# Kernel tuning notes

Hardware: AMD Instinct MI355X
Metric: run time of the kernel (lower is better)

## Reference

```python
import jax, jax.numpy as jnp
import numpy as np

N = 20000      # nodes
E = 640000     # edges
FIN = 256
FQK = 256


def setup_inputs() -> dict:
    key = jax.random.key(0)
    kx, ks, kd, kw = jax.random.split(key, 4)
    x = jax.random.normal(kx, (N, FIN), dtype=jnp.float32)
    # src must be sorted (original scatter_softmax assumes grouped index);
    # force last element to N-1 so nbatches == N as in batch[-1]+1.
    src = jnp.sort(jax.random.randint(ks, (E,), 0, N))
    src = src.at[-1].set(N - 1)
    dest = jax.random.randint(kd, (E,), 0, N)
    ei = jnp.stack([src, dest]).astype(jnp.int64)
    # nn.Linear(Fin, 2*Fqk, bias=False) weight: [2*Fqk, Fin]
    bound = 1.0 / np.sqrt(FIN)
    W = jax.random.uniform(kw, (2 * FQK, FIN), dtype=jnp.float32,
                           minval=-bound, maxval=bound)
    return {"x": x, "ei": ei, "W": W}


def reference(x, ei, W):
    src, dest = ei[0], ei[1]
    n_nodes = x.shape[0]
    scaling = FQK ** -0.5
    qk = x @ W.T                      # [N, 2*Fqk]
    q, k = jnp.split(qk, 2, axis=-1)  # each [N, Fqk]
    q = q * scaling
    # per-edge dot product: (q[src] . k[dest])  -> [E]
    aw = jnp.einsum('ef,ef->e', q[src], k[dest])
    # scatter softmax over edges grouped by src node (raw exp, as original)
    ex = jnp.exp(aw)
    expsum = jax.ops.segment_sum(ex, src, num_segments=n_nodes)  # [N]
    return ex / expsum[src]
```

## Files before the change

kernel.cpp:

```cpp
#include <hip/hip_runtime.h>
#include <cmath>

#define FIN 256
#define FQK 256
#define SCALING 0.0625f
#define MAX_SEG 256

typedef __bf16 bf16_t;
typedef bf16_t bf16x8 __attribute__((ext_vector_type(8)));
typedef float  f32x4  __attribute__((ext_vector_type(4)));

__device__ __forceinline__ unsigned short f2bf(float f) {
    unsigned int u = __float_as_uint(f);
    u += 0x7FFFu + ((u >> 16) & 1u);
    return (unsigned short)(u >> 16);
}
__device__ __forceinline__ float bf_lo(unsigned int w) { return __uint_as_float(w << 16); }
__device__ __forceinline__ float bf_hi(unsigned int w) { return __uint_as_float(w & 0xFFFF0000u); }
__device__ __forceinline__ unsigned int pack2(float a, float b) {
    return (unsigned int)f2bf(a) | ((unsigned int)f2bf(b) << 16);
}

__global__ __launch_bounds__(256) void prep_wb_kernel(const float* __restrict__ W,
                                                      unsigned int* __restrict__ Wb2) {
    const int i = blockIdx.x * 256 + threadIdx.x;
    const float4 v = *(const float4*)(W + (size_t)i * 4);
    uint2 p;
    p.x = pack2(v.x, v.y);
    p.y = pack2(v.z, v.w);
    *(uint2*)(Wb2 + (size_t)i * 2) = p;
}

#define GROWS    32
#define SAROW    264

__global__ __launch_bounds__(256) void gemm_qk_kernel(const float* __restrict__ x,
                                                      const unsigned short* __restrict__ Wb,
                                                      unsigned short* __restrict__ qarr,
                                                      unsigned short* __restrict__ karr,
                                                      int N) {
    __shared__ unsigned short sA[GROWS * SAROW];

    const int h    = blockIdx.y;
    const unsigned short* __restrict__ Wbh = Wb + (size_t)h * FQK * FIN;
    unsigned short* __restrict__ outp = h ? karr : qarr;
    const float scale = h ? 1.0f : SCALING;

    const int t    = threadIdx.x;
    const int wv   = t >> 6;
    const int lane = t & 63;
    const int q    = lane >> 4;
    const int m16  = lane & 15;
    const int n0   = blockIdx.x * GROWS;
    const int f0   = wv * 64;

    uint4 bfrag[4][8];
#pragma unroll
    for (int ft = 0; ft < 4; ++ft) {
        const unsigned short* __restrict__ brow = Wbh + (size_t)(f0 + ft * 16 + m16) * FIN;
#pragma unroll
        for (int kc = 0; kc < 8; ++kc)
            bfrag[ft][kc] = *(const uint4*)(brow + kc * 32 + q * 8);
    }

    {
        const int r  = t >> 6;
        const int c4 = (t & 63) * 4;
#pragma unroll
        for (int u = 0; u < 8; ++u) {
            const int row = u * 4 + r;
            const int n = n0 + row;
            float4 v = make_float4(0.f, 0.f, 0.f, 0.f);
            if (n < N) v = *(const float4*)(x + (size_t)n * FIN + c4);
            uint2 p;
            p.x = pack2(v.x, v.y);
            p.y = pack2(v.z, v.w);
            *(uint2*)&sA[row * SAROW + c4] = p;
        }
    }
    __syncthreads();

    f32x4 acc[2][4] = {};
#pragma unroll
    for (int kc = 0; kc < 8; ++kc) {
        bf16x8 afrag[2];
#pragma unroll
        for (int mt = 0; mt < 2; ++mt)
            afrag[mt] = *(const bf16x8*)&sA[(mt * 16 + m16) * SAROW + kc * 32 + q * 8];
#pragma unroll
        for (int ft = 0; ft < 4; ++ft) {
            union { uint4 u; bf16x8 v; } bu;
            bu.u = bfrag[ft][kc];
#pragma unroll
            for (int mt = 0; mt < 2; ++mt)
                acc[mt][ft] = __builtin_amdgcn_mfma_f32_16x16x32_bf16(afrag[mt], bu.v,
                                                                     acc[mt][ft], 0, 0, 0);
        }
    }

#pragma unroll
    for (int mt = 0; mt < 2; ++mt) {
#pragma unroll
        for (int r = 0; r < 4; ++r) {
            const int n = n0 + mt * 16 + q * 4 + r;
            if (n < N) {
#pragma unroll
                for (int ft = 0; ft < 4; ++ft)
                    outp[(size_t)n * FIN + f0 + ft * 16 + m16] = f2bf(acc[mt][ft][r] * scale);
            }
        }
    }
}

__global__ __launch_bounds__(256) void seg_kernel(const int* __restrict__ src,
                                                  int* __restrict__ seg, int N, int E) {
    const int n = blockIdx.x * 256 + threadIdx.x;
    if (n > N) return;
    int lo = 0, hi = E;
    while (lo < hi) {
        const int mid = (lo + hi) >> 1;
        if (src[mid] < n) lo = mid + 1; else hi = mid;
    }
    seg[n] = lo;
}

__global__ __launch_bounds__(256) void node_edge_kernel(const unsigned short* __restrict__ qarr,
                                                        const unsigned short* __restrict__ karr,
                                                        const int* __restrict__ dest,
                                                        const int* __restrict__ seg,
                                                        float* __restrict__ out, int N) {
    __shared__ float exlds[4][MAX_SEG];

    const int w    = threadIdx.x >> 6;
    const int lane = threadIdx.x & 63;
    const int n    = blockIdx.x * 4 + w;
    const int g    = lane >> 4;
    const int j    = lane & 15;

    int   s0 = 0, cnt = 0;
    float inv = 0.f;

    if (n < N) {
        s0 = seg[n];
        cnt = seg[n + 1] - s0;
    }

    if (cnt > 0) {
        const uint4* __restrict__ qr = (const uint4*)(qarr + (size_t)n * FIN);
        const uint4 qa0 = qr[j];
        const uint4 qa1 = qr[16 + j];
        float4 xa, xb, xc, xd;
        xa.x = bf_lo(qa0.x); xa.y = bf_hi(qa0.x); xa.z = bf_lo(qa0.y); xa.w = bf_hi(qa0.y);
        xb.x = bf_lo(qa0.z); xb.y = bf_hi(qa0.z); xb.z = bf_lo(qa0.w); xb.w = bf_hi(qa0.w);
        xc.x = bf_lo(qa1.x); xc.y = bf_hi(qa1.x); xc.z = bf_lo(qa1.y); xc.w = bf_hi(qa1.y);
        xd.x = bf_lo(qa1.z); xd.y = bf_hi(qa1.z); xd.z = bf_lo(qa1.w); xd.w = bf_hi(qa1.w);

        float sum = 0.f;
        for (int base = 0; base < cnt; base += 64) {
            const int m = min(64, cnt - base);
            const int vd = (lane < m) ? dest[s0 + base + lane] : 0;
            const int nit = (m + 3) >> 2;
            for (int it = 0; it < nit; it += 2) {
                const int  eg0 = it * 4 + g;
                const int  eg1 = eg0 + 4;
                const bool v0  = eg0 < m;
                const bool v1  = eg1 < m;
                const int  d0  = __shfl(vd, eg0, 64);
                const int  d1  = __shfl(vd, eg1, 64);
                const uint4* __restrict__ kr0 = (const uint4*)(karr + (size_t)(v0 ? d0 : 0) * FIN);
                const uint4* __restrict__ kr1 = (const uint4*)(karr + (size_t)(v1 ? d1 : 0) * FIN);
                const uint4 q00 = kr0[j];
                const uint4 q01 = kr0[16 + j];
                const uint4 q10 = kr1[j];
                const uint4 q11 = kr1[16 + j];

                float a0 = 0.f, a1 = 0.f;
                a0 += bf_lo(q00.x) * xa.x + bf_hi(q00.x) * xa.y
                    + bf_lo(q00.y) * xa.z + bf_hi(q00.y) * xa.w
                    + bf_lo(q00.z) * xb.x + bf_hi(q00.z) * xb.y
                    + bf_lo(q00.w) * xb.z + bf_hi(q00.w) * xb.w;
                a0 += bf_lo(q01.x) * xc.x + bf_hi(q01.x) * xc.y
                    + bf_lo(q01.y) * xc.z + bf_hi(q01.y) * xc.w
                    + bf_lo(q01.z) * xd.x + bf_hi(q01.z) * xd.y
                    + bf_lo(q01.w) * xd.z + bf_hi(q01.w) * xd.w;
                a1 += bf_lo(q10.x) * xa.x + bf_hi(q10.x) * xa.y
                    + bf_lo(q10.y) * xa.z + bf_hi(q10.y) * xa.w
                    + bf_lo(q10.z) * xb.x + bf_hi(q10.z) * xb.y
                    + bf_lo(q10.w) * xb.z + bf_hi(q10.w) * xb.w;
                a1 += bf_lo(q11.x) * xc.x + bf_hi(q11.x) * xc.y
                    + bf_lo(q11.y) * xc.z + bf_hi(q11.y) * xc.w
                    + bf_lo(q11.z) * xd.x + bf_hi(q11.z) * xd.y
                    + bf_lo(q11.w) * xd.z + bf_hi(q11.w) * xd.w;

                a0 += __shfl_xor(a0, 1, 64);
                a1 += __shfl_xor(a1, 1, 64);
                a0 += __shfl_xor(a0, 2, 64);
                a1 += __shfl_xor(a1, 2, 64);
                a0 += __shfl_xor(a0, 4, 64);
                a1 += __shfl_xor(a1, 4, 64);
                a0 += __shfl_xor(a0, 8, 64);
                a1 += __shfl_xor(a1, 8, 64);

                if (v0) {
                    const float ex = __expf(a0);
                    sum += ex;
                    const int idx = base + eg0;
                    if (j == 0 && idx < MAX_SEG) exlds[w][idx] = ex;
                }
                if (v1) {
                    const float ex = __expf(a1);
                    sum += ex;
                    const int idx = base + eg1;
                    if (j == 0 && idx < MAX_SEG) exlds[w][idx] = ex;
                }
            }
        }
        sum += __shfl_xor(sum, 16, 64);
        sum += __shfl_xor(sum, 32, 64);
        inv = 1.0f / sum;
    }

    __syncthreads();

    if (cnt > 0) {
        const int lim = cnt < MAX_SEG ? cnt : MAX_SEG;
        for (int i = lane; i < lim; i += 64)
            out[s0 + i] = exlds[w][i] * inv;
    }
}

extern "C" void kernel_launch(void* const* d_in, const int* in_sizes, int n_in,
                              void* d_out, int out_size, void* d_ws, size_t ws_size,
                              hipStream_t stream) {
    const float* x  = (const float*)d_in[0];
    const int*   ei = (const int*)d_in[1];
    const float* W  = (const float*)d_in[2];
    float* out = (float*)d_out;

    const int N = in_sizes[0] / FIN;
    const int E = in_sizes[1] / 2;

    unsigned short* qarr = (unsigned short*)d_ws;
    unsigned short* karr = qarr + (size_t)N * FIN;
    unsigned short* Wb   = karr + (size_t)N * FIN;
    int*            seg  = (int*)(Wb + (size_t)2 * FQK * FIN);

    prep_wb_kernel<<<(2 * FQK * FIN) / (256 * 4), 256, 0, stream>>>(W, (unsigned int*)Wb);

    dim3 ggrid((N + GROWS - 1) / GROWS, 2);
    gemm_qk_kernel<<<ggrid, 256, 0, stream>>>(x, Wb, qarr, karr, N);

    seg_kernel<<<(N + 256) / 256, 256, 0, stream>>>(ei, seg, N, E);

    node_edge_kernel<<<(N + 3) / 4, 256, 0, stream>>>(qarr, karr, ei + E, seg, out, N);
}
```

Before: 140.6 us.

## Split edge dot products across feature chunks and add separate softmax finalize

The per-edge q·k dot product is split into four 64-feature chunks, each handled by its own grid slice. Partial dots go to a workspace buffer, and a new finalize kernel sums them, applies exp and normalizes per source segment. The prep kernel also takes over the segment binary search, and the GEMM now preloads its A fragments while streaming B per feature tile instead of holding all of B in registers. This adds parallelism and cuts register pressure, at the cost of extra global traffic for the partial dots and one more launch.

```diff
diff --git a/kernel.cpp b/kernel.cpp
--- a/kernel.cpp
+++ b/kernel.cpp
@@ -5,6 +5,7 @@
 #define FQK 256
 #define SCALING 0.0625f
 #define MAX_SEG 256
+#define NCHUNK 4
 
 typedef __bf16 bf16_t;
 typedef bf16_t bf16x8 __attribute__((ext_vector_type(8)));
@@ -21,14 +22,29 @@
     return (unsigned int)f2bf(a) | ((unsigned int)f2bf(b) << 16);
 }
 
-__global__ __launch_bounds__(256) void prep_wb_kernel(const float* __restrict__ W,
-                                                      unsigned int* __restrict__ Wb2) {
-    const int i = blockIdx.x * 256 + threadIdx.x;
-    const float4 v = *(const float4*)(W + (size_t)i * 4);
-    uint2 p;
-    p.x = pack2(v.x, v.y);
-    p.y = pack2(v.z, v.w);
-    *(uint2*)(Wb2 + (size_t)i * 2) = p;
+__global__ __launch_bounds__(256) void prep_kernel(const float* __restrict__ W,
+                                                   uint2* __restrict__ Wb2,
+                                                   const int* __restrict__ src,
+                                                   int* __restrict__ seg, int N, int E) {
+    const int b = blockIdx.x;
+    if (b < 128) {
+        const int i = b * 256 + threadIdx.x;
+        const float4 v = ((const float4*)W)[i];
+        uint2 p;
+        p.x = pack2(v.x, v.y);
+        p.y = pack2(v.z, v.w);
+        Wb2[i] = p;
+    } else {
+        const int n = (b - 128) * 256 + threadIdx.x;
+        if (n <= N) {
+            int lo = 0, hi = E;
+            while (lo < hi) {
+                const int mid = (lo + hi) >> 1;
+                if (src[mid] < n) lo = mid + 1; else hi = mid;
+            }
+            seg[n] = lo;
+        }
+    }
 }
 
 #define GROWS    32
@@ -53,15 +69,6 @@
     const int m16  = lane & 15;
     const int n0   = blockIdx.x * GROWS;
     const int f0   = wv * 64;
-
-    uint4 bfrag[4][8];
-#pragma unroll
-    for (int ft = 0; ft < 4; ++ft) {
-        const unsigned short* __restrict__ brow = Wbh + (size_t)(f0 + ft * 16 + m16) * FIN;
-#pragma unroll
-        for (int kc = 0; kc < 8; ++kc)
-            bfrag[ft][kc] = *(const uint4*)(brow + kc * 32 + q * 8);
-    }
 
     {
         const int r  = t >> 6;
@@ -80,20 +87,28 @@
     }
     __syncthreads();
 
+    bf16x8 afrag[2][8];
+#pragma unroll
+    for (int mt = 0; mt < 2; ++mt)
+#pragma unroll
+        for (int kc = 0; kc < 8; ++kc)
+            afrag[mt][kc] = *(const bf16x8*)&sA[(mt * 16 + m16) * SAROW + kc * 32 + q * 8];
+
     f32x4 acc[2][4] = {};
 #pragma unroll
-    for (int kc = 0; kc < 8; ++kc) {
-        bf16x8 afrag[2];
-#pragma unroll
-        for (int mt = 0; mt < 2; ++mt)
-            afrag[mt] = *(const bf16x8*)&sA[(mt * 16 + m16) * SAROW + kc * 32 + q * 8];
-#pragma unroll
-        for (int ft = 0; ft < 4; ++ft) {
+    for (int ft = 0; ft < 4; ++ft) {
+        const uint4* __restrict__ brow =
+            (const uint4*)(Wbh + (size_t)(f0 + ft * 16 + m16) * FIN);
+        uint4 bfr[8];
+#pragma unroll
+        for (int kc = 0; kc < 8; ++kc) bfr[kc] = brow[kc * 4 + q];
+#pragma unroll
+        for (int kc = 0; kc < 8; ++kc) {
             union { uint4 u; bf16x8 v; } bu;
-            bu.u = bfrag[ft][kc];
+            bu.u = bfr[kc];
 #pragma unroll
             for (int mt = 0; mt < 2; ++mt)
-                acc[mt][ft] = __builtin_amdgcn_mfma_f32_16x16x32_bf16(afrag[mt], bu.v,
+                acc[mt][ft] = __builtin_amdgcn_mfma_f32_16x16x32_bf16(afrag[mt][kc], bu.v,
                                                                      acc[mt][ft], 0, 0, 0);
         }
     }
@@ -112,121 +127,97 @@
     }
 }
 
-__global__ __launch_bounds__(256) void seg_kernel(const int* __restrict__ src,
-                                                  int* __restrict__ seg, int N, int E) {
-    const int n = blockIdx.x * 256 + threadIdx.x;
-    if (n > N) return;
-    int lo = 0, hi = E;
-    while (lo < hi) {
-        const int mid = (lo + hi) >> 1;
-        if (src[mid] < n) lo = mid + 1; else hi = mid;
-    }
-    seg[n] = lo;
-}
-
-__global__ __launch_bounds__(256) void node_edge_kernel(const unsigned short* __restrict__ qarr,
+__global__ __launch_bounds__(256) void chunk_dot_kernel(const unsigned short* __restrict__ qarr,
                                                         const unsigned short* __restrict__ karr,
                                                         const int* __restrict__ dest,
                                                         const int* __restrict__ seg,
-                                                        float* __restrict__ out, int N) {
-    __shared__ float exlds[4][MAX_SEG];
-
+                                                        float* __restrict__ pdot,
+                                                        int N, int E) {
+    __shared__ float plds[4][MAX_SEG];
+
+    const int c    = blockIdx.y;
     const int w    = threadIdx.x >> 6;
     const int lane = threadIdx.x & 63;
     const int n    = blockIdx.x * 4 + w;
     const int g    = lane >> 4;
     const int j    = lane & 15;
 
-    int   s0 = 0, cnt = 0;
-    float inv = 0.f;
-
+    int s0 = 0, cnt = 0;
     if (n < N) {
         s0 = seg[n];
         cnt = seg[n + 1] - s0;
     }
-
-    if (cnt > 0) {
-        const uint4* __restrict__ qr = (const uint4*)(qarr + (size_t)n * FIN);
-        const uint4 qa0 = qr[j];
-        const uint4 qa1 = qr[16 + j];
-        float4 xa, xb, xc, xd;
-        xa.x = bf_lo(qa0.x); xa.y = bf_hi(qa0.x); xa.z = bf_lo(qa0.y); xa.w = bf_hi(qa0.y);
-        xb.x = bf_lo(qa0.z); xb.y = bf_hi(qa0.z); xb.z = bf_lo(qa0.w); xb.w = bf_hi(qa0.w);
-        xc.x = bf_lo(qa1.x); xc.y = bf_hi(qa1.x); xc.z = bf_lo(qa1.y); xc.w = bf_hi(qa1.y);
-        xd.x = bf_lo(qa1.z); xd.y = bf_hi(qa1.z); xd.z = bf_lo(qa1.w); xd.w = bf_hi(qa1.w);
-
-        float sum = 0.f;
-        for (int base = 0; base < cnt; base += 64) {
-            const int m = min(64, cnt - base);
-            const int vd = (lane < m) ? dest[s0 + base + lane] : 0;
-            const int nit = (m + 3) >> 2;
-            for (int it = 0; it < nit; it += 2) {
-                const int  eg0 = it * 4 + g;
-                const int  eg1 = eg0 + 4;
-                const bool v0  = eg0 < m;
-                const bool v1  = eg1 < m;
-                const int  d0  = __shfl(vd, eg0, 64);
-                const int  d1  = __shfl(vd, eg1, 64);
-                const uint4* __restrict__ kr0 = (const uint4*)(karr + (size_t)(v0 ? d0 : 0) * FIN);
-                const uint4* __restrict__ kr1 = (const uint4*)(karr + (size_t)(v1 ? d1 : 0) * FIN);
-                const uint4 q00 = kr0[j];
-                const uint4 q01 = kr0[16 + j];
-                const uint4 q10 = kr1[j];
-                const uint4 q11 = kr1[16 + j];
-
-                float a0 = 0.f, a1 = 0.f;
-                a0 += bf_lo(q00.x) * xa.x + bf_hi(q00.x) * xa.y
-                    + bf_lo(q00.y) * xa.z + bf_hi(q00.y) * xa.w
-                    + bf_lo(q00.z) * xb.x + bf_hi(q00.z) * xb.y
-                    + bf_lo(q00.w) * xb.z + bf_hi(q00.w) * xb.w;
-                a0 += bf_lo(q01.x) * xc.x + bf_hi(q01.x) * xc.y
-                    + bf_lo(q01.y) * xc.z + bf_hi(q01.y) * xc.w
-                    + bf_lo(q01.z) * xd.x + bf_hi(q01.z) * xd.y
-                    + bf_lo(q01.w) * xd.z + bf_hi(q01.w) * xd.w;
-                a1 += bf_lo(q10.x) * xa.x + bf_hi(q10.x) * xa.y
-                    + bf_lo(q10.y) * xa.z + bf_hi(q10.y) * xa.w
-                    + bf_lo(q10.z) * xb.x + bf_hi(q10.z) * xb.y
-                    + bf_lo(q10.w) * xb.z + bf_hi(q10.w) * xb.w;
-                a1 += bf_lo(q11.x) * xc.x + bf_hi(q11.x) * xc.y
-                    + bf_lo(q11.y) * xc.z + bf_hi(q11.y) * xc.w
-                    + bf_lo(q11.z) * xd.x + bf_hi(q11.z) * xd.y
-                    + bf_lo(q11.w) * xd.z + bf_hi(q11.w) * xd.w;
-
-                a0 += __shfl_xor(a0, 1, 64);
-                a1 += __shfl_xor(a1, 1, 64);
-                a0 += __shfl_xor(a0, 2, 64);
-                a1 += __shfl_xor(a1, 2, 64);
-                a0 += __shfl_xor(a0, 4, 64);
-                a1 += __shfl_xor(a1, 4, 64);
-                a0 += __shfl_xor(a0, 8, 64);
-                a1 += __shfl_xor(a1, 8, 64);
-
-                if (v0) {
-                    const float ex = __expf(a0);
-                    sum += ex;
-                    const int idx = base + eg0;
-                    if (j == 0 && idx < MAX_SEG) exlds[w][idx] = ex;
+    if (cnt <= 0) return;
+
+    const uint2 qc = ((const uint2*)(qarr + (size_t)n * FIN))[c * 16 + j];
+    const float qx0 = bf_lo(qc.x), qx1 = bf_hi(qc.x);
+    const float qx2 = bf_lo(qc.y), qx3 = bf_hi(qc.y);
+
+    for (int base = 0; base < cnt; base += 64) {
+        const int m = min(64, cnt - base);
+        const int vd = (lane < m) ? dest[s0 + base + lane] : 0;
+        const int nit = (m + 15) >> 4;
+        for (int it = 0; it < nit; ++it) {
+            const int e0 = it * 16 + g * 4;
+            int dd[4];
+#pragma unroll
+            for (int u = 0; u < 4; ++u) dd[u] = __shfl(vd, e0 + u, 64);
+            uint2 kv[4];
+#pragma unroll
+            for (int u = 0; u < 4; ++u)
+                kv[u] = ((const uint2*)(karr +
+                          (size_t)((e0 + u < m) ? dd[u] : 0) * FIN))[c * 16 + j];
+            float dot[4];
+#pragma unroll
+            for (int u = 0; u < 4; ++u)
+                dot[u] = bf_lo(kv[u].x) * qx0 + bf_hi(kv[u].x) * qx1
+                       + bf_lo(kv[u].y) * qx2 + bf_hi(kv[u].y) * qx3;
+#pragma unroll
+            for (int st = 1; st <= 8; st <<= 1) {
+#pragma unroll
+                for (int u = 0; u < 4; ++u)
+                    dot[u] += __shfl_xor(dot[u], st, 64);
+            }
+            if (j == 0) {
+#pragma unroll
+                for (int u = 0; u < 4; ++u) {
+                    const int idx = base + e0 + u;
+                    if (e0 + u < m && idx < MAX_SEG) plds[w][idx] = dot[u];
                 }
-                if (v1) {
-                    const float ex = __expf(a1);
-                    sum += ex;
-                    const int idx = base + eg1;
-                    if (j == 0 && idx < MAX_SEG) exlds[w][idx] = ex;
-                }
-            }
-        }
-        sum += __shfl_xor(sum, 16, 64);
-        sum += __shfl_xor(sum, 32, 64);
-        inv = 1.0f / sum;
-    }
-
-    __syncthreads();
-
-    if (cnt > 0) {
-        const int lim = cnt < MAX_SEG ? cnt : MAX_SEG;
-        for (int i = lane; i < lim; i += 64)
-            out[s0 + i] = exlds[w][i] * inv;
-    }
+            }
+        }
+    }
+
+    float* __restrict__ pc = pdot + (size_t)c * E;
+    const int lim = cnt < MAX_SEG ? cnt : MAX_SEG;
+    for (int i = lane; i < lim; i += 64) pc[s0 + i] = plds[w][i];
+}
+
+__global__ __launch_bounds__(256) void finalize_kernel(const float* __restrict__ pdot,
+                                                       const int* __restrict__ seg,
+                                                       float* __restrict__ out,
+                                                       int N, int E) {
+    const int w    = threadIdx.x >> 6;
+    const int lane = threadIdx.x & 63;
+    const int n    = blockIdx.x * 4 + w;
+    if (n >= N) return;
+    const int s0  = seg[n];
+    const int cnt = seg[n + 1] - s0;
+    if (cnt <= 0) return;
+
+    float sum = 0.f;
+    for (int i = lane; i < cnt; i += 64) {
+        const size_t e = (size_t)(s0 + i);
+        const float aw = pdot[e] + pdot[(size_t)E + e]
+                       + pdot[2 * (size_t)E + e] + pdot[3 * (size_t)E + e];
+        const float ex = __expf(aw);
+        out[e] = ex;
+        sum += ex;
+    }
+#pragma unroll
+    for (int st = 1; st <= 32; st <<= 1) sum += __shfl_xor(sum, st, 64);
+    const float inv = 1.0f / sum;
+    for (int i = lane; i < cnt; i += 64) out[s0 + i] *= inv;
 }
 
 extern "C" void kernel_launch(void* const* d_in, const int* in_sizes, int n_in,
@@ -243,14 +234,16 @@
     unsigned short* qarr = (unsigned short*)d_ws;
     unsigned short* karr = qarr + (size_t)N * FIN;
     unsigned short* Wb   = karr + (size_t)N * FIN;
-    int*            seg  = (int*)(Wb + (size_t)2 * FQK * FIN);
-
-    prep_wb_kernel<<<(2 * FQK * FIN) / (256 * 4), 256, 0, stream>>>(W, (unsigned int*)Wb);
+    float*          pdot = (float*)(Wb + (size_t)2 * FQK * FIN);
+    int*            seg  = (int*)(pdot + (size_t)NCHUNK * E);
+
+    prep_kernel<<<128 + (N + 256) / 256, 256, 0, stream>>>(W, (uint2*)Wb, ei, seg, N, E);
 
     dim3 ggrid((N + GROWS - 1) / GROWS, 2);
     gemm_qk_kernel<<<ggrid, 256, 0, stream>>>(x, Wb, qarr, karr, N);
 
-    seg_kernel<<<(N + 256) / 256, 256, 0, stream>>>(ei, seg, N, E);
-
-    node_edge_kernel<<<(N + 3) / 4, 256, 0, stream>>>(qarr, karr, ei + E, seg, out, N);
-}
+    dim3 cgrid((N + 3) / 4, NCHUNK);
+    chunk_dot_kernel<<<cgrid, 256, 0, stream>>>(qarr, karr, ei + E, seg, pdot, N, E);
+
+    finalize_kernel<<<(N + 3) / 4, 256, 0, stream>>>(pdot, seg, out, N, E);
+}
```

New measurement: 166.3 us. 1.18x slower.
